# Optimization experiments

Measured on AMD Instinct MI355X. Metric: run time of the kernel, lower is better.

The kernel has to match this reference:

```python
import jax, jax.numpy as jnp
import numpy as np

SIGMA = 2.5
B, L, V, C = 8, 2048, 8192, 64
F = 2 * (C + 1)  # top_net in_features = 130


def rbf_interp(points_1, feats_1, points_2, sigma):
    """RBF interpolation of feats_1 at points_1 onto points_2 (atom2D torch_rbf, concat=True).
    points_1: [V,3], feats_1: [V,C], points_2: [L,3] -> [L, C+1]
    """
    # exact cdist via gram trick, [L, V]
    d2 = (jnp.sum(points_2 * points_2, -1)[:, None]
          - 2.0 * (points_2 @ points_1.T)
          + jnp.sum(points_1 * points_1, -1)[None, :])
    d = jnp.sqrt(jnp.maximum(d2, 0.0))
    w = jnp.exp(-d / sigma)                       # [L, V]
    dens = jnp.sum(w, axis=1, keepdims=True)      # [L, 1]
    w = w / dens
    # original computes weights under torch.no_grad()
    w = jax.lax.stop_gradient(w)
    dens = jax.lax.stop_gradient(dens)
    feats_2 = w @ feats_1                         # [L, C]
    return jnp.concatenate([feats_2, dens], axis=1)


def setup_inputs() -> dict:
    key = jax.random.key(0)
    ks = jax.random.split(key, 8)
    return {
        "locs_left": jax.random.normal(ks[0], (B, L, 3), jnp.float32),
        "locs_right": jax.random.normal(ks[1], (B, L, 3), jnp.float32),
        "verts_left": jax.random.normal(ks[2], (B, V, 3), jnp.float32),
        "verts_right": jax.random.normal(ks[3], (B, V, 3), jnp.float32),
        "feats_left": jax.random.normal(ks[4], (B, V, C), jnp.float32),
        "feats_right": jax.random.normal(ks[5], (B, V, C), jnp.float32),
        "w1": jax.random.normal(ks[6], (F, F), jnp.float32) * (1.0 / np.sqrt(F)),
        "b1": jnp.zeros((F,), jnp.float32),
        "w2": jax.random.normal(ks[7], (1, F), jnp.float32) * (1.0 / np.sqrt(F)),
        "b2": jnp.zeros((1,), jnp.float32),
    }


def reference(locs_left, locs_right, verts_left, verts_right,
              feats_left, feats_right, w1, b1, w2, b2):
    interp = jax.vmap(lambda p1, f1, p2: rbf_interp(p1, f1, p2, SIGMA))
    fl = interp(verts_left, feats_left, locs_left)     # [B, L, C+1]
    fr = interp(verts_right, feats_right, locs_right)  # [B, L, C+1]
    x = jnp.concatenate([fl, fr], axis=-1)             # [B, L, 2*(C+1)]
    h = jax.nn.relu(x @ w1.T + b1)                     # dropout inactive at eval
    out = h @ w2.T + b2                                # [B, L, 1]
    return out.reshape(-1)                             # [B*L]
```

## Files before the change

### kernel.cpp

```cpp
#include <hip/hip_runtime.h>
#include <hip/hip_bf16.h>
#include <stdint.h>

#define B_ 8
#define L_ 2048
#define V_ 8192
#define C_ 64
#define F_ 130

typedef float    f32x4  __attribute__((ext_vector_type(4)));
typedef float    f32x2  __attribute__((ext_vector_type(2)));
typedef short    s16x8  __attribute__((ext_vector_type(8)));
typedef __bf16   bf16x8 __attribute__((ext_vector_type(8)));
typedef uint32_t u32x4  __attribute__((ext_vector_type(4)));

#if __has_builtin(__builtin_amdgcn_exp2f)
#define EXP2(x) __builtin_amdgcn_exp2f(x)
#else
#define EXP2(x) exp2f(x)
#endif

#if __has_builtin(__builtin_elementwise_fma)
#define PK_FMA4(a,b,c) __builtin_elementwise_fma((a),(b),(c))
#else
__device__ __forceinline__ f32x4 PK_FMA4(f32x4 a, f32x4 b, f32x4 c) {
  f32x4 r; for (int i=0;i<4;++i) r[i]=fmaf(a[i],b[i],c[i]); return r;
}
#endif
#if __has_builtin(__builtin_elementwise_max)
#define PK_MAX4(a,b) __builtin_elementwise_max((a),(b))
#else
__device__ __forceinline__ f32x4 PK_MAX4(f32x4 a, f32x4 b) {
  f32x4 r; for (int i=0;i<4;++i) r[i]=fmaxf(a[i],b[i]); return r;
}
#endif

constexpr float KEXP2 = (float)(0.57707801635558535 * 0.57707801635558535);

__device__ __forceinline__ uint32_t pack2bf(float a, float b) {
  uint16_t ua = __builtin_bit_cast(uint16_t, (__bf16)a);
  uint16_t ub = __builtin_bit_cast(uint16_t, (__bf16)b);
  return (uint32_t)ua | ((uint32_t)ub << 16);
}

__device__ __forceinline__ float wave_sum(float v) {
  v += __shfl_xor(v, 1);  v += __shfl_xor(v, 2);  v += __shfl_xor(v, 4);
  v += __shfl_xor(v, 8);  v += __shfl_xor(v, 16); v += __shfl_xor(v, 32);
  return v;
}

__device__ __forceinline__ void gload_lds16(const void* g, void* l) {
  __builtin_amdgcn_global_load_lds(
      (const __attribute__((address_space(1))) void*)g,
      (__attribute__((address_space(3))) void*)l, 16, 0, 0);
}

__global__ __launch_bounds__(256) void pre_kernel(
    const float* __restrict__ verts_l, const float* __restrict__ verts_r,
    const float* __restrict__ feats_l, const float* __restrict__ feats_r,
    uint16_t* __restrict__ fT2, float* __restrict__ vS2)
{
  __shared__ float fs[64][68];
  const int blk = blockIdx.x, tid = threadIdx.x;
  if (blk < 1024) {
    const int p = blk >> 6, kt2 = blk & 63;
    const int side = p >> 3, bb = p & 7;
    const float* src = (side ? feats_r : feats_l) + (size_t)bb * (V_ * C_);
    const int r  = tid & 63;
    const int eq = tid >> 6;
    const int ch = r >> 3;
    const int kq = (r & 7) ^ (ch & 7);
    #pragma unroll
    for (int sub = 0; sub < 2; ++sub) {
      const int ktile = kt2 * 2 + sub;
      const int v0 = ktile * 64;
      {
        const int sv = tid >> 2, c0 = (tid & 3) * 16;
        const int m = ((sv >> 3) & 7) << 3;
        const float* s = src + (size_t)(v0 + sv) * C_ + c0;
        f32x4 a = *(const f32x4*)(s);
        f32x4 b = *(const f32x4*)(s + 4);
        f32x4 c = *(const f32x4*)(s + 8);
        f32x4 d = *(const f32x4*)(s + 12);
        *(f32x4*)&fs[sv][(c0)      ^ m] = a;
        *(f32x4*)&fs[sv][(c0 + 4)  ^ m] = b;
        *(f32x4*)&fs[sv][(c0 + 8)  ^ m] = c;
        *(f32x4*)&fs[sv][(c0 + 12) ^ m] = d;
      }
      __syncthreads();
      {
        const int e = eq * 2;
        const int row0 = kq * 8 + e;
        const int mm = kq << 3;
        const float f0 = fs[row0][ch ^ mm];
        const float f1 = fs[row0 + 1][ch ^ mm];
        char* dst = (char*)fT2 + ((size_t)p * 128 + ktile) * 8192 + r * 16 + eq * 4;
        *(uint32_t*)dst = pack2bf(f0, f1);
      }
      __syncthreads();
    }
  } else {
    const int blk2 = blk - 1024;
    const int p = blk2 >> 5, chunk = blk2 & 31;
    const int side = p >> 3, bb = p & 7;
    const float* src = (side ? verts_r : verts_l) + (size_t)bb * (V_ * 3);
    const int v = chunk * 256 + tid;
    const float x = src[v * 3 + 0], y = src[v * 3 + 1], z = src[v * 3 + 2];
    const float n2 = x * x + y * y + z * z;
    constexpr float M2K = -2.0f * KEXP2;
    float* d = vS2 + (size_t)p * 32768 + (size_t)(v >> 6) * 256 + (v & 63);
    d[0] = M2K * x; d[64] = M2K * y; d[128] = M2K * z; d[192] = KEXP2 * n2;
  }
}

__global__ __launch_bounds__(512, 4) void fused_kernel(
    const float* __restrict__ locs_l, const float* __restrict__ locs_r,
    const uint16_t* __restrict__ fT2, const float* __restrict__ vS2,
    const float* __restrict__ w1, const float* __restrict__ b1,
    const float* __restrict__ w2, const float* __restrict__ b2,
    float* __restrict__ outp)
{
  __shared__ __align__(16) char  flds[2][16384];
  __shared__ __align__(16) float vlds[2][2][4][64];
  __shared__ __align__(16) float xs[32][136];
  __shared__ float densp[32];

  const int bid  = blockIdx.x;
  const int bb   = bid & 7;
  const int tile = bid >> 3;
  const int tid  = threadIdx.x;
  const int wid  = tid >> 6, lane = tid & 63;
  const int g    = wid & 1, h = wid >> 1;
  const int ln15 = lane & 15, lg = lane >> 4;
  const int xorv = (ln15 & 7) << 4;
  const f32x4 zero4 = {0.f, 0.f, 0.f, 0.f};

  const int sub  = h >> 1;
  const int hh   = h & 1;
  const int abfix = sub * 8192 + ln15 * 128 + ((((hh << 2) | lg) << 4) ^ xorv);

  for (int s = 0; s < 2; ++s) {
    const int p = s * 8 + bb;
    const float* locs = (s ? locs_r : locs_l) + (size_t)bb * (L_ * 3);
    const int arow = tile * 32 + g * 16 + ln15;
    const float px = locs[arow * 3 + 0];
    const float py = locs[arow * 3 + 1];
    const float pz = locs[arow * 3 + 2];
    const float pn2p = KEXP2 * (px * px + py * py + pz * pz);
    const f32x4 px4 = {px, px, px, px};
    const f32x4 py4 = {py, py, py, py};
    const f32x4 pz4 = {pz, pz, pz, pz};
    const f32x4 pn4 = {pn2p, pn2p, pn2p, pn2p};

    const char* ftp = (const char*)fT2 + (size_t)p * (128 * 8192);
    const char* vtp = (const char*)vS2 + (size_t)p * (128 * 1024);

    f32x4 acc0 = zero4, acc1 = zero4, acc2 = zero4, acc3 = zero4;
    f32x4 densa = zero4;

    gload_lds16(ftp + wid * 2048 + lane * 16,        &flds[0][wid * 2048]);
    gload_lds16(ftp + wid * 2048 + 1024 + lane * 16, &flds[0][wid * 2048 + 1024]);
    if (wid < 2) gload_lds16(vtp + wid * 1024 + lane * 16, &vlds[0][wid][0][0]);
    __syncthreads();

    for (int kt = 0; kt < 64; ++kt) {
      const int cur = kt & 1;
      if (kt < 63) {
        const int nxt = cur ^ 1;
        const char* gf = ftp + (size_t)(kt + 1) * 16384 + wid * 2048;
        gload_lds16(gf + lane * 16,        &flds[nxt][wid * 2048]);
        gload_lds16(gf + 1024 + lane * 16, &flds[nxt][wid * 2048 + 1024]);
        if (wid < 2)
          gload_lds16(vtp + (size_t)(kt + 1) * 2048 + wid * 1024 + lane * 16,
                      &vlds[nxt][wid][0][0]);
      }
      const int kof = hh * 32 + lg * 8;
      const f32x4 vxa = *(const f32x4*)&vlds[cur][sub][0][kof];
      const f32x4 vxb = *(const f32x4*)&vlds[cur][sub][0][kof + 4];
      const f32x4 vya = *(const f32x4*)&vlds[cur][sub][1][kof];
      const f32x4 vyb = *(const f32x4*)&vlds[cur][sub][1][kof + 4];
      const f32x4 vza = *(const f32x4*)&vlds[cur][sub][2][kof];
      const f32x4 vzb = *(const f32x4*)&vlds[cur][sub][2][kof + 4];
      const f32x4 vna = *(const f32x4*)&vlds[cur][sub][3][kof];
      const f32x4 vnb = *(const f32x4*)&vlds[cur][sub][3][kof + 4];

      f32x4 d2a = PK_FMA4(vza, pz4, vna + pn4);
      d2a = PK_FMA4(vya, py4, d2a);
      d2a = PK_FMA4(vxa, px4, d2a);
      d2a = PK_MAX4(d2a, zero4);
      f32x4 d2b = PK_FMA4(vzb, pz4, vnb + pn4);
      d2b = PK_FMA4(vyb, py4, d2b);
      d2b = PK_FMA4(vxb, px4, d2b);
      d2b = PK_MAX4(d2b, zero4);

      f32x4 wa, wb;
      #pragma unroll
      for (int e = 0; e < 4; ++e) {
        wa[e] = EXP2(-__builtin_amdgcn_sqrtf(d2a[e]));
        wb[e] = EXP2(-__builtin_amdgcn_sqrtf(d2b[e]));
      }
      densa += wa;
      densa += wb;
      bf16x8 av;
      #pragma unroll
      for (int e = 0; e < 4; ++e) {
        av[e]     = (__bf16)wa[e];
        av[e + 4] = (__bf16)wb[e];
      }
      const s16x8 afrag = __builtin_bit_cast(s16x8, av);
      const char* fl = flds[cur];
      const s16x8 bf0 = *(const s16x8*)(fl + abfix);
      const s16x8 bf1 = *(const s16x8*)(fl + abfix + 2048);
      const s16x8 bf2 = *(const s16x8*)(fl + abfix + 4096);
      const s16x8 bf3 = *(const s16x8*)(fl + abfix + 6144);
      acc0 = __builtin_amdgcn_mfma_f32_16x16x32_bf16(afrag, bf0, acc0, 0, 0, 0);
      acc1 = __builtin_amdgcn_mfma_f32_16x16x32_bf16(afrag, bf1, acc1, 0, 0, 0);
      acc2 = __builtin_amdgcn_mfma_f32_16x16x32_bf16(afrag, bf2, acc2, 0, 0, 0);
      acc3 = __builtin_amdgcn_mfma_f32_16x16x32_bf16(afrag, bf3, acc3, 0, 0, 0);
      __syncthreads();
    }

    float dens = (densa.x + densa.y) + (densa.z + densa.w);
    dens += __shfl_xor(dens, 16);
    dens += __shfl_xor(dens, 32);

    #pragma unroll
    for (int ph = 0; ph < 4; ++ph) {
      if (h == ph) {
        if (ph == 0) {
          if (lane < 16) densp[g * 16 + lane] = dens;
          #pragma unroll
          for (int r = 0; r < 4; ++r) {
            const int row = g * 16 + lg * 4 + r;
            xs[row][s * 65 +      ln15] = acc0[r];
            xs[row][s * 65 + 16 + ln15] = acc1[r];
            xs[row][s * 65 + 32 + ln15] = acc2[r];
            xs[row][s * 65 + 48 + ln15] = acc3[r];
          }
        } else {
          if (lane < 16) densp[g * 16 + lane] += dens;
          #pragma unroll
          for (int r = 0; r < 4; ++r) {
            const int row = g * 16 + lg * 4 + r;
            xs[row][s * 65 +      ln15] += acc0[r];
            xs[row][s * 65 + 16 + ln15] += acc1[r];
            xs[row][s * 65 + 32 + ln15] += acc2[r];
            xs[row][s * 65 + 48 + ln15] += acc3[r];
          }
        }
      }
      __syncthreads();
    }
    for (int idx = tid; idx < 32 * 64; idx += 512) {
      const int row = idx >> 6, c = idx & 63;
      xs[row][s * 65 + c] *= (1.0f / densp[row]);
    }
    if (tid < 32) xs[tid][s * 65 + 64] = densp[tid];
    __syncthreads();
  }

  const int r0 = wid * 4;
  float hh0[4] = {0.f,0.f,0.f,0.f}, hh1[4] = {0.f,0.f,0.f,0.f};
  const float* wr0 = w1 + (size_t)lane * F_;
  const float* wr1 = w1 + (size_t)(lane + 64) * F_;

  #pragma unroll 4
  for (int i = 0; i < 128; i += 4) {
    const f32x2 a01 = *(const f32x2*)&wr0[i];
    const f32x2 a23 = *(const f32x2*)&wr0[i + 2];
    const f32x2 c01 = *(const f32x2*)&wr1[i];
    const f32x2 c23 = *(const f32x2*)&wr1[i + 2];
    #pragma unroll
    for (int r = 0; r < 4; ++r) {
      const f32x4 xv = *(const f32x4*)&xs[r0 + r][i];
      hh0[r] = fmaf(xv.x, a01.x, hh0[r]); hh0[r] = fmaf(xv.y, a01.y, hh0[r]);
      hh0[r] = fmaf(xv.z, a23.x, hh0[r]); hh0[r] = fmaf(xv.w, a23.y, hh0[r]);
      hh1[r] = fmaf(xv.x, c01.x, hh1[r]); hh1[r] = fmaf(xv.y, c01.y, hh1[r]);
      hh1[r] = fmaf(xv.z, c23.x, hh1[r]); hh1[r] = fmaf(xv.w, c23.y, hh1[r]);
    }
  }
  {
    const float a0 = wr0[128], a1 = wr0[129];
    const float c0 = wr1[128], c1 = wr1[129];
    #pragma unroll
    for (int r = 0; r < 4; ++r) {
      const float x0 = xs[r0 + r][128], x1 = xs[r0 + r][129];
      hh0[r] = fmaf(x0, a0, fmaf(x1, a1, hh0[r]));
      hh1[r] = fmaf(x0, c0, fmaf(x1, c1, hh1[r]));
    }
  }
  const float* wr2 = w1 + 128 * F_;
  const float* wr3 = w1 + 129 * F_;
  float hp2[4], hp3[4];
  #pragma unroll
  for (int r = 0; r < 4; ++r) {
    const float xa = xs[r0 + r][lane];
    const float xb = xs[r0 + r][lane + 64];
    float p2 = wr2[lane] * xa + wr2[lane + 64] * xb;
    float p3 = wr3[lane] * xa + wr3[lane + 64] * xb;
    if (lane < 2) {
      const float xc = xs[r0 + r][128 + lane];
      p2 += wr2[128 + lane] * xc;
      p3 += wr3[128 + lane] * xc;
    }
    hp2[r] = wave_sum(p2);
    hp3[r] = wave_sum(p3);
  }
  const float b1a = b1[lane], b1b = b1[lane + 64];
  const float w2a = w2[lane], w2b = w2[lane + 64];
  const float b1c = b1[128], b1d = b1[129];
  const float w2c = w2[128], w2d = w2[129];
  const float b2v = b2[0];
  #pragma unroll
  for (int r = 0; r < 4; ++r) {
    float o = w2a * fmaxf(hh0[r] + b1a, 0.f) + w2b * fmaxf(hh1[r] + b1b, 0.f);
    o = wave_sum(o);
    if (lane == 0) {
      o += w2c * fmaxf(hp2[r] + b1c, 0.f) + w2d * fmaxf(hp3[r] + b1d, 0.f);
      outp[(size_t)bb * L_ + tile * 32 + r0 + r] = o + b2v;
    }
  }
}

extern "C" void kernel_launch(void* const* d_in, const int* in_sizes, int n_in,
                              void* d_out, int out_size, void* d_ws, size_t ws_size,
                              hipStream_t stream) {
  const float* locs_l  = (const float*)d_in[0];
  const float* locs_r  = (const float*)d_in[1];
  const float* verts_l = (const float*)d_in[2];
  const float* verts_r = (const float*)d_in[3];
  const float* feats_l = (const float*)d_in[4];
  const float* feats_r = (const float*)d_in[5];
  const float* w1 = (const float*)d_in[6];
  const float* b1 = (const float*)d_in[7];
  const float* w2 = (const float*)d_in[8];
  const float* b2 = (const float*)d_in[9];

  char* ws = (char*)d_ws;
  uint16_t* fT2 = (uint16_t*)ws;
  float*    vS2 = (float*)(ws + 16777216);
  float*    out = (float*)d_out;

  pre_kernel<<<1536, 256, 0, stream>>>(verts_l, verts_r, feats_l, feats_r, fT2, vS2);
  fused_kernel<<<512, 512, 0, stream>>>(locs_l, locs_r, fT2, vS2,
                                        w1, b1, w2, b2, out);
}
```

Baseline: 223.8 us.

## Vectorize feature transpose stores, raise occupancy hint, trim LDS padding, hoist prefetch pointers

The pre-kernel transpose now has each thread gather eight rows and emit one 16-byte store per row group instead of 4-byte stores, which cuts store instruction count. The fused kernel's launch bounds raise the minimum-blocks hint from 4 to 6, pushing the compiler toward fewer registers so more waves are resident. The xs padding shrinks from 136 to 132 columns, which lowers LDS use per block. Prefetch addresses become incrementing pointers so the loop does less address arithmetic. The tighter register budget risks spills, and the new padding may change LDS bank conflicts.

```diff
diff --git a/kernel.cpp b/kernel.cpp
--- a/kernel.cpp
+++ b/kernel.cpp
@@ -66,10 +66,6 @@
     const int p = blk >> 6, kt2 = blk & 63;
     const int side = p >> 3, bb = p & 7;
     const float* src = (side ? feats_r : feats_l) + (size_t)bb * (V_ * C_);
-    const int r  = tid & 63;
-    const int eq = tid >> 6;
-    const int ch = r >> 3;
-    const int kq = (r & 7) ^ (ch & 7);
     #pragma unroll
     for (int sub = 0; sub < 2; ++sub) {
       const int ktile = kt2 * 2 + sub;
@@ -89,13 +85,21 @@
       }
       __syncthreads();
       {
-        const int e = eq * 2;
-        const int row0 = kq * 8 + e;
-        const int mm = kq << 3;
-        const float f0 = fs[row0][ch ^ mm];
-        const float f1 = fs[row0 + 1][ch ^ mm];
-        char* dst = (char*)fT2 + ((size_t)p * 128 + ktile) * 8192 + r * 16 + eq * 4;
-        *(uint32_t*)dst = pack2bf(f0, f1);
+        char* tb = (char*)fT2 + ((size_t)p * 128 + ktile) * 8192;
+        #pragma unroll
+        for (int half = 0; half < 2; ++half) {
+          const int r  = half * 256 + tid;
+          const int ch = r >> 3;
+          const int kq = (r & 7) ^ (ch & 7);
+          const int cs = ch ^ (kq << 3);
+          const int row0 = kq * 8;
+          float f[8];
+          #pragma unroll
+          for (int e = 0; e < 8; ++e) f[e] = fs[row0 + e][cs];
+          u32x4 val = { pack2bf(f[0], f[1]), pack2bf(f[2], f[3]),
+                        pack2bf(f[4], f[5]), pack2bf(f[6], f[7]) };
+          *(u32x4*)(tb + r * 16) = val;
+        }
       }
       __syncthreads();
     }
@@ -113,7 +117,7 @@
   }
 }
 
-__global__ __launch_bounds__(512, 4) void fused_kernel(
+__global__ __launch_bounds__(512, 6) void fused_kernel(
     const float* __restrict__ locs_l, const float* __restrict__ locs_r,
     const uint16_t* __restrict__ fT2, const float* __restrict__ vS2,
     const float* __restrict__ w1, const float* __restrict__ b1,
@@ -122,7 +126,7 @@
 {
   __shared__ __align__(16) char  flds[2][16384];
   __shared__ __align__(16) float vlds[2][2][4][64];
-  __shared__ __align__(16) float xs[32][136];
+  __shared__ __align__(16) float xs[32][132];
   __shared__ float densp[32];
 
   const int bid  = blockIdx.x;
@@ -163,16 +167,18 @@
     if (wid < 2) gload_lds16(vtp + wid * 1024 + lane * 16, &vlds[0][wid][0][0]);
     __syncthreads();
 
+    const char* gfn = ftp + 16384 + wid * 2048 + lane * 16;
+    const char* gvn = vtp + 2048  + wid * 1024 + lane * 16;
+
     for (int kt = 0; kt < 64; ++kt) {
       const int cur = kt & 1;
       if (kt < 63) {
         const int nxt = cur ^ 1;
-        const char* gf = ftp + (size_t)(kt + 1) * 16384 + wid * 2048;
-        gload_lds16(gf + lane * 16,        &flds[nxt][wid * 2048]);
-        gload_lds16(gf + 1024 + lane * 16, &flds[nxt][wid * 2048 + 1024]);
-        if (wid < 2)
-          gload_lds16(vtp + (size_t)(kt + 1) * 2048 + wid * 1024 + lane * 16,
-                      &vlds[nxt][wid][0][0]);
+        gload_lds16(gfn,        &flds[nxt][wid * 2048]);
+        gload_lds16(gfn + 1024, &flds[nxt][wid * 2048 + 1024]);
+        if (wid < 2) gload_lds16(gvn, &vlds[nxt][wid][0][0]);
+        gfn += 16384;
+        gvn += 2048;
       }
       const int kof = hh * 32 + lg * 8;
       const f32x4 vxa = *(const f32x4*)&vlds[cur][sub][0][kof];
```

New measurement: 226.0 us. About the same (+1.0%).
